# Kernel tuning notes

Hardware: AMD Instinct MI355X
Metric: run time of the kernel (lower is better)

## Reference

```python
import jax, jax.numpy as jnp
import numpy as np

L = 2          # num_blocks
E = 256        # embed_features
FIN = 64       # input_features
FF = 4 * E     # dim_feedforward
OUT = 10       # out_dim
WCTX = 64      # context_len
B, S = 2, 1024
LN_EPS = 1e-5


def _ln(x, g, b):
    m = jnp.mean(x, axis=-1, keepdims=True)
    v = jnp.mean((x - m) ** 2, axis=-1, keepdims=True)
    return (x - m) / jnp.sqrt(v + LN_EPS) * g + b


def setup_inputs() -> dict:
    key = jax.random.key(0)
    ks = jax.random.split(key, 12)
    s = 0.02
    return {
        "inputs": jax.random.normal(ks[0], (B, S, FIN), jnp.float32),
        "embed_w": jax.random.normal(ks[1], (E, FIN), jnp.float32) * s,
        "embed_b": jnp.zeros((E,), jnp.float32),
        "qkv_w": jax.random.normal(ks[2], (L, 3 * E, E), jnp.float32) * s,
        "qkv_b": jnp.zeros((L, 3 * E), jnp.float32),
        "attn_out_w": jax.random.normal(ks[3], (L, E, E), jnp.float32) * s,
        "attn_out_b": jnp.zeros((L, E), jnp.float32),
        "ln1_g": jnp.ones((L, E), jnp.float32),
        "ln1_b": jnp.zeros((L, E), jnp.float32),
        "ffn1_w": jax.random.normal(ks[4], (L, FF, E), jnp.float32) * s,
        "ffn1_b": jnp.zeros((L, FF), jnp.float32),
        "ffn2_w": jax.random.normal(ks[5], (L, E, FF), jnp.float32) * s,
        "ffn2_b": jnp.zeros((L, E), jnp.float32),
        "ln2_g": jnp.ones((L, E), jnp.float32),
        "ln2_b": jnp.zeros((L, E), jnp.float32),
        "head_w": jax.random.normal(ks[6], (OUT, E), jnp.float32) * s,
        "head_b": jnp.zeros((OUT,), jnp.float32),
        "context_len": WCTX,
    }


def reference(inputs, embed_w, embed_b, qkv_w, qkv_b, attn_out_w, attn_out_b,
              ln1_g, ln1_b, ffn1_w, ffn1_b, ffn2_w, ffn2_b, ln2_g, ln2_b,
              head_w, head_b, context_len):
    b, s, _ = inputs.shape
    e = embed_w.shape[0]
    nh = max(1, e // 64) * 2           # torch: nhead = max(1, E//64)*2
    hd = e // nh
    scale = 1.0 / np.sqrt(hd)
    w = context_len

    emb = inputs @ embed_w.T + embed_b                       # [B,S,E]
    # left-pad with W-1 zeros so window pos p = padded[p:p+W] (zeros for early pos)
    padded = jnp.pad(emb, ((0, 0), (w - 1, 0), (0, 0)))
    idx = jnp.arange(s)[:, None] + jnp.arange(w)[None, :]    # [S,W]
    x = padded[:, idx].reshape(b * s, w, e)                  # [B*S,W,E]

    nlayers = qkv_w.shape[0]
    for l in range(nlayers):
        qkv = x @ qkv_w[l].T + qkv_b[l]                      # [N,W,3E]
        q, k, v = jnp.split(qkv, 3, axis=-1)
        q = q.reshape(-1, w, nh, hd)
        k = k.reshape(-1, w, nh, hd)
        v = v.reshape(-1, w, nh, hd)
        scores = jnp.einsum('nqhd,nkhd->nhqk', q, k) * scale
        attn = jax.nn.softmax(scores, axis=-1)
        o = jnp.einsum('nhqk,nkhd->nqhd', attn, v).reshape(-1, w, e)
        o = o @ attn_out_w[l].T + attn_out_b[l]
        x = _ln(x + o, ln1_g[l], ln1_b[l])                   # post-norm (torch default)
        ff = jax.nn.silu(x @ ffn1_w[l].T + ffn1_b[l]) @ ffn2_w[l].T + ffn2_b[l]
        x = _ln(x + ff, ln2_g[l], ln2_b[l])

    out = x[:, -1, :] @ head_w.T + head_b                    # last token of each window
    return out.reshape(b, s, -1)
```

## Files before the change

kernel.cpp:

```cpp
#include <hip/hip_runtime.h>
#include <hip/hip_bf16.h>

#define BB_ 2
#define SS_ 1024
#define FIN_ 64
#define EE_ 256
#define FF_ 1024
#define NH_ 8
#define HD_ 32
#define OUT_ 10
#define NWIN (BB_ * SS_)
#define NT 512
#define SCALE_ 0.17677669529663687f
#define XBP 264
#define TPAD 1088

typedef unsigned short u16;
typedef unsigned int u32;
typedef __attribute__((ext_vector_type(8))) short bf8_t;
typedef __attribute__((ext_vector_type(4))) float f4_t;
#define MFMA_B16(a, b, c) __builtin_amdgcn_mfma_f32_16x16x32_bf16(a, b, c, 0, 0, 0)

__device__ __forceinline__ u16 bf16r(float f) {
    u32 u = __builtin_bit_cast(u32, f);
    return (u16)((u + 0x7FFFu + ((u >> 16) & 1u)) >> 16);
}
__device__ __forceinline__ u32 pk_bf16(float a, float b) {
    return (u32)bf16r(a) | ((u32)bf16r(b) << 16);
}
__device__ __forceinline__ float b2f(u16 h) {
    return __builtin_bit_cast(float, ((u32)h) << 16);
}
__device__ __forceinline__ float b2f_lo(u32 u) {
    return __builtin_bit_cast(float, u << 16);
}
__device__ __forceinline__ float b2f_hi(u32 u) {
    return __builtin_bit_cast(float, u & 0xFFFF0000u);
}

__device__ __forceinline__ float dot4(float4 a, float4 b) {
    return a.x * b.x + a.y * b.y + a.z * b.z + a.w * b.w;
}
__device__ __forceinline__ float wsum(float v) {
#pragma unroll
    for (int o = 32; o > 0; o >>= 1) v += __shfl_xor(v, o, 64);
    return v;
}
__device__ __forceinline__ float wmax(float v) {
#pragma unroll
    for (int o = 32; o > 0; o >>= 1) v = fmaxf(v, __shfl_xor(v, o, 64));
    return v;
}
__device__ __forceinline__ float silu_f(float h) { return h / (1.f + __expf(-h)); }

struct CvtArgs {
    const float* s[9];
    u16* d[9];
    int n[9];
};

__global__ void k_pre(const float* __restrict__ in, const float* __restrict__ embw,
                      const float* __restrict__ embb, const float* __restrict__ qkv_b,
                      CvtArgs ca, float* __restrict__ emb, u16* __restrict__ qkvp) {
    __shared__ float row[FIN_];
    const int blk = blockIdx.x;
    const int tid = threadIdx.x;
    if (blk < 2048) {
        if (tid < FIN_) row[tid] = in[blk * FIN_ + tid];
        __syncthreads();
        const float4* w4 = (const float4*)(embw + tid * FIN_);
        const float4* r4 = (const float4*)row;
        float s = 0.f;
#pragma unroll
        for (int c = 0; c < FIN_ / 4; ++c) s += dot4(w4[c], r4[c]);
        emb[blk * EE_ + tid] = s + embb[tid];
    } else if (blk < 2816) {
        const int b2 = blk - 2048;
#pragma unroll 1
        for (int seg = 0; seg < 9; ++seg) {
            const float* __restrict__ src = ca.s[seg];
            u16* __restrict__ dst = ca.d[seg];
            const int nn = ca.n[seg];
            for (int i = b2 * 256 + tid; i < nn; i += 768 * 256)
                dst[i] = bf16r(src[i]);
        }
    } else {
        const int b3 = blk - 2816;
        for (int f = b3 * 256 + tid; f < 2 * 64 * 768; f += 8 * 256) {
            const int bat = f / 49152;
            const int rem = f - bat * 49152;
            const int r = rem / 768, cl = rem - r * 768;
            qkvp[((size_t)bat * TPAD + r) * 768 + cl] = bf16r(qkv_b[cl]);
        }
    }
}

__global__ __launch_bounds__(512) void k_qkv0m(const float* __restrict__ emb,
                                               const u16* __restrict__ wq0b,
                                               const float* __restrict__ qkvb,
                                               u16* __restrict__ qkvp) {
    __shared__ u16 ab[16 * XBP];
    const int b = blockIdx.x;
    const int tid = threadIdx.x, lane = tid & 63, wv = tid >> 6;
    const int col = lane & 15, quad = lane >> 4;
    for (int idx = tid; idx < 16 * 256; idx += 512) {
        const int i = idx >> 8, e = idx & 255;
        ab[i * XBP + e] = bf16r(emb[(b * 16 + i) * EE_ + e]);
    }
    __syncthreads();
    f4_t acc[6];
#pragma unroll
    for (int nt = 0; nt < 6; ++nt) acc[nt] = (f4_t){0.f, 0.f, 0.f, 0.f};
#pragma unroll
    for (int ks = 0; ks < 8; ++ks) {
        const bf8_t ax = *(const bf8_t*)(ab + col * XBP + ks * 32 + quad * 8);
#pragma unroll
        for (int nt = 0; nt < 6; ++nt) {
            const int r = wv * 96 + nt * 16 + col;
            const bf8_t bw = *(const bf8_t*)(wq0b + r * EE_ + ks * 32 + quad * 8);
            acc[nt] = MFMA_B16(ax, bw, acc[nt]);
        }
    }
#pragma unroll
    for (int nt = 0; nt < 6; ++nt) {
        const int cc = wv * 96 + nt * 16 + col;
        const float bs = qkvb[cc];
#pragma unroll
        for (int j = 0; j < 4; ++j) {
            const int tok = b * 16 + quad * 4 + j;
            const int bb = tok >> 10;
            const size_t ti = (size_t)bb * TPAD + (tok & 1023) + 64;
            qkvp[ti * 768 + cc] = bf16r(acc[nt][j] + bs);
        }
    }
}

__device__ __forceinline__ void reg_ln(float (&x)[2][4][4], float* red, float* stat,
                                       u16* xb,
                                       float gc0, float gc1, float bc0, float bc1,
                                       int tid, int wv, int col, int quad,
                                       int colg0, int colg1) {
    float ps[4][4], pq[4][4];
#pragma unroll
    for (int mt = 0; mt < 4; ++mt)
#pragma unroll
        for (int j = 0; j < 4; ++j) {
            const float v0 = x[0][mt][j], v1 = x[1][mt][j];
            ps[mt][j] = v0 + v1;
            pq[mt][j] = v0 * v0 + v1 * v1;
        }
#pragma unroll
    for (int o = 1; o < 16; o <<= 1) {
#pragma unroll
        for (int mt = 0; mt < 4; ++mt)
#pragma unroll
            for (int j = 0; j < 4; ++j) {
                ps[mt][j] += __shfl_xor(ps[mt][j], o);
                pq[mt][j] += __shfl_xor(pq[mt][j], o);
            }
    }
    if (col == 0) {
#pragma unroll
        for (int mt = 0; mt < 4; ++mt)
#pragma unroll
            for (int j = 0; j < 4; ++j) {
                const int row = mt * 16 + quad * 4 + j;
                red[row * 17 + wv * 2] = ps[mt][j];
                red[row * 17 + wv * 2 + 1] = pq[mt][j];
            }
    }
    __syncthreads();
    if (tid < 64) {
        float s = 0.f, q = 0.f;
#pragma unroll
        for (int w = 0; w < 8; ++w) {
            s += red[tid * 17 + w * 2];
            q += red[tid * 17 + w * 2 + 1];
        }
        const float m = s * 0.00390625f;
        const float var = q * 0.00390625f - m * m;
        stat[tid * 2] = m;
        stat[tid * 2 + 1] = rsqrtf(var + 1e-5f);
    }
    __syncthreads();
#pragma unroll
    for (int mt = 0; mt < 4; ++mt)
#pragma unroll
        for (int j = 0; j < 4; ++j) {
            const int row = mt * 16 + quad * 4 + j;
            const float m = stat[row * 2];
            const float rs = stat[row * 2 + 1];
            const float xn0 = (x[0][mt][j] - m) * rs * gc0 + bc0;
            const float xn1 = (x[1][mt][j] - m) * rs * gc1 + bc1;
            x[0][mt][j] = xn0;
            x[1][mt][j] = xn1;
            const u32 w = pk_bf16(xn0, xn1);
            xb[row * XBP + colg0] = (u16)w;
            xb[row * XBP + colg1] = (u16)(w >> 16);
        }
}

struct __align__(16) SMemA {
    union {
        struct { u16 qkpb[9216]; u16 vt[4608]; } att;
        struct { float red[64 * 17]; float stat[128]; } ln;
    } r1;
    u16 obxb[64 * XBP];
};

__global__ __launch_bounds__(NT, 4) void k_attn(
    const float* __restrict__ emb, const u16* __restrict__ qkvp,
    const u16* __restrict__ wob, const float* __restrict__ aob,
    const float* __restrict__ ln1g, const float* __restrict__ ln1b,
    u16* __restrict__ xbg) {
    __shared__ SMemA sm;
    const int n = blockIdx.x;
    const int bb = n >> 10, p = n & 1023;
    const int tid = threadIdx.x;
    const int lane = tid & 63, wv = tid >> 6;
    const int col = lane & 15, quad = lane >> 4;
    const int colg0 = wv * 32 + col, colg1 = colg0 + 16;

    for (int hp = 0; hp < 4; ++hp) {
        {
            const int i = tid >> 3, dg = tid & 7;
            const size_t rb = ((size_t)bb * TPAD + (p + 1 + i)) * 768 + hp * 64 + dg * 8;
            const uint4 q4 = *(const uint4*)(qkvp + rb);
            const uint4 k4 = *(const uint4*)(qkvp + rb + 256);
            const uint4 v4 = *(const uint4*)(qkvp + rb + 512);
            *(uint4*)(sm.r1.att.qkpb + i * 72 + dg * 8) = q4;
            *(uint4*)(sm.r1.att.qkpb + 4608 + i * 72 + dg * 8) = k4;
            union { uint4 u; u16 h[8]; } vu; vu.u = v4;
#pragma unroll
            for (int c = 0; c < 8; ++c)
                sm.r1.att.vt[(dg * 8 + c) * 72 + i] = vu.h[c];
        }
        __syncthreads();
        const int hh = wv >> 2, mt_ = wv & 3;
        const int r0 = mt_ * 16 + quad * 4;
        const bf8_t aq = *(const bf8_t*)(sm.r1.att.qkpb + (mt_ * 16 + col) * 72 + hh * 32 + quad * 8);
        f4_t sc[4];
#pragma unroll
        for (int nt = 0; nt < 4; ++nt) {
            const bf8_t bk = *(const bf8_t*)(sm.r1.att.qkpb + 4608 + (nt * 16 + col) * 72 + hh * 32 + quad * 8);
            f4_t z = {0.f, 0.f, 0.f, 0.f};
            sc[nt] = MFMA_B16(aq, bk, z);
        }
#pragma unroll
        for (int j = 0; j < 4; ++j) {
            float s0 = sc[0][j] * SCALE_, s1 = sc[1][j] * SCALE_;
            float s2v = sc[2][j] * SCALE_, s3 = sc[3][j] * SCALE_;
            float m = fmaxf(fmaxf(s0, s1), fmaxf(s2v, s3));
            m = fmaxf(m, __shfl_xor(m, 1)); m = fmaxf(m, __shfl_xor(m, 2));
            m = fmaxf(m, __shfl_xor(m, 4)); m = fmaxf(m, __shfl_xor(m, 8));
            const float e0 = __expf(s0 - m), e1 = __expf(s1 - m);
            const float e2 = __expf(s2v - m), e3 = __expf(s3 - m);
            float s = e0 + e1 + e2 + e3;
            s += __shfl_xor(s, 1); s += __shfl_xor(s, 2);
            s += __shfl_xor(s, 4); s += __shfl_xor(s, 8);
            const float inv = 1.f / s;
            sc[0][j] = e0 * inv; sc[1][j] = e1 * inv;
            sc[2][j] = e2 * inv; sc[3][j] = e3 * inv;
        }
        __syncthreads();
        u16* pbh = sm.r1.att.qkpb + hh * 4608;
#pragma unroll
        for (int nt = 0; nt < 4; ++nt) {
            const u32 w01 = pk_bf16(sc[nt][0], sc[nt][1]);
            const u32 w23 = pk_bf16(sc[nt][2], sc[nt][3]);
            u16* pp = pbh + r0 * 72 + nt * 16 + col;
            pp[0] = (u16)w01; pp[72] = (u16)(w01 >> 16);
            pp[144] = (u16)w23; pp[216] = (u16)(w23 >> 16);
        }
        f4_t ov[2];
        ov[0] = (f4_t){0.f, 0.f, 0.f, 0.f}; ov[1] = (f4_t){0.f, 0.f, 0.f, 0.f};
#pragma unroll
        for (int ks = 0; ks < 2; ++ks) {
            const bf8_t ap = *(const bf8_t*)(pbh + (mt_ * 16 + col) * 72 + ks * 32 + quad * 8);
#pragma unroll
            for (int ntl = 0; ntl < 2; ++ntl) {
                const bf8_t bv = *(const bf8_t*)(sm.r1.att.vt +
                                                 (hh * 32 + ntl * 16 + col) * 72 + ks * 32 + quad * 8);
                ov[ntl] = MFMA_B16(ap, bv, ov[ntl]);
            }
        }
#pragma unroll
        for (int ntl = 0; ntl < 2; ++ntl) {
            const u32 w01 = pk_bf16(ov[ntl][0], ov[ntl][1]);
            const u32 w23 = pk_bf16(ov[ntl][2], ov[ntl][3]);
            u16* oo = sm.obxb + r0 * XBP + (hp * 2 + hh) * 32 + ntl * 16 + col;
            oo[0] = (u16)w01; oo[XBP] = (u16)(w01 >> 16);
            oo[2 * XBP] = (u16)w23; oo[3 * XBP] = (u16)(w23 >> 16);
        }
        __syncthreads();
    }

    f4_t pacc[2][4];
#pragma unroll
    for (int a = 0; a < 2; ++a)
#pragma unroll
        for (int m = 0; m < 4; ++m) pacc[a][m] = (f4_t){0.f, 0.f, 0.f, 0.f};
#pragma unroll 2
    for (int ks = 0; ks < 8; ++ks) {
        bf8_t ao[4];
#pragma unroll
        for (int mt = 0; mt < 4; ++mt)
            ao[mt] = *(const bf8_t*)(sm.obxb + (mt * 16 + col) * XBP + ks * 32 + quad * 8);
#pragma unroll
        for (int ntl = 0; ntl < 2; ++ntl) {
            const bf8_t bw = *(const bf8_t*)(wob + ((wv * 2 + ntl) * 16 + col) * EE_ +
                                             ks * 32 + quad * 8);
#pragma unroll
            for (int mt = 0; mt < 4; ++mt) pacc[ntl][mt] = MFMA_B16(ao[mt], bw, pacc[ntl][mt]);
        }
    }

    const float aob_0 = aob[colg0], aob_1 = aob[colg1];
    float x[2][4][4];
#pragma unroll
    for (int mt = 0; mt < 4; ++mt)
#pragma unroll
        for (int j = 0; j < 4; ++j) {
            const int row = mt * 16 + quad * 4 + j;
            const int t = p - 63 + row;
            const size_t base = (size_t)((bb << 10) + t) * EE_;
            const float e0 = (t >= 0) ? emb[base + colg0] : 0.f;
            const float e1 = (t >= 0) ? emb[base + colg1] : 0.f;
            x[0][mt][j] = e0 + aob_0 + pacc[0][mt][j];
            x[1][mt][j] = e1 + aob_1 + pacc[1][mt][j];
        }
    __syncthreads();
    reg_ln(x, sm.r1.ln.red, sm.r1.ln.stat, sm.obxb,
           ln1g[colg0], ln1g[colg1], ln1b[colg0], ln1b[colg1],
           tid, wv, col, quad, colg0, colg1);
    __syncthreads();
    u16* dst = xbg + (size_t)n * 64 * 256;
#pragma unroll
    for (int k = 0; k < 4; ++k) {
        const int idx = tid + k * NT;
        const int row = idx >> 5, seg = idx & 31;
        *(uint4*)(dst + row * 256 + seg * 8) = *(const uint4*)(sm.obxb + row * XBP + seg * 8);
    }
}

struct __align__(16) SMemB {
    u16 xb[64 * XBP];
    union {
        u16 hb[64 * 136];
        struct { u16 k1[64 * 66]; u16 v1[64 * 66]; } kv;
        struct { float red[64 * 17]; float stat[128]; } ln;
    } c;
    float x1row[256];
    float o1b[256];
    float q1b[64];
    float sbuf2[128];
};

__global__ __launch_bounds__(NT, 4) void k_mlp(
    const u16* __restrict__ xbg,
    const u16* __restrict__ w1b, const u16* __restrict__ w2b,
    const u16* __restrict__ wkvb, const u16* __restrict__ wq1b,
    const u16* __restrict__ wob1,
    const float* __restrict__ qkv_b, const float* __restrict__ aob,
    const float* __restrict__ f1b, const float* __restrict__ f2b,
    const float* __restrict__ ln2g, const float* __restrict__ ln2b,
    float* __restrict__ x2g) {
    __shared__ SMemB sm;
    const int n = blockIdx.x;
    const int tid = threadIdx.x;
    const int lane = tid & 63, wv = tid >> 6;
    const int col = lane & 15, quad = lane >> 4;
    const int colg0 = wv * 32 + col, colg1 = colg0 + 16;

    const float* qkv_b1 = qkv_b + 3 * EE_;
    const float* aob1p = aob + EE_;

    const u16* src = xbg + (size_t)n * 64 * 256;
#pragma unroll
    for (int k = 0; k < 4; ++k) {
        const int idx = tid + k * NT;
        const int row = idx >> 5, seg = idx & 31;
        *(uint4*)(sm.xb + row * XBP + seg * 8) = *(const uint4*)(src + row * 256 + seg * 8);
    }
    __syncthreads();

    f4_t facc[2][4];
#pragma unroll
    for (int a = 0; a < 2; ++a)
#pragma unroll
        for (int m = 0; m < 4; ++m) facc[a][m] = (f4_t){0.f, 0.f, 0.f, 0.f};

    for (int c = 0; c < 8; ++c) {
        {
            f4_t hacc[4];
#pragma unroll
            for (int m = 0; m < 4; ++m) hacc[m] = (f4_t){0.f, 0.f, 0.f, 0.f};
            const int f = c * 128 + wv * 16 + col;
#pragma unroll 2
            for (int ks = 0; ks < 8; ++ks) {
                const bf8_t bw = *(const bf8_t*)(w1b + f * EE_ + ks * 32 + quad * 8);
#pragma unroll
                for (int mt = 0; mt < 4; ++mt) {
                    const bf8_t axr = *(const bf8_t*)(sm.xb + (mt * 16 + col) * XBP + ks * 32 + quad * 8);
                    hacc[mt] = MFMA_B16(axr, bw, hacc[mt]);
                }
            }
            const float bv = f1b[f];
            const int lc = wv * 16 + col;
#pragma unroll
            for (int mt = 0; mt < 4; ++mt) {
                const u32 w01 = pk_bf16(silu_f(hacc[mt][0] + bv), silu_f(hacc[mt][1] + bv));
                const u32 w23 = pk_bf16(silu_f(hacc[mt][2] + bv), silu_f(hacc[mt][3] + bv));
                u16* hh2 = sm.c.hb + (mt * 16 + quad * 4) * 136 + lc;
                hh2[0] = (u16)w01; hh2[136] = (u16)(w01 >> 16);
                hh2[272] = (u16)w23; hh2[408] = (u16)(w23 >> 16);
            }
        }
        __syncthreads();
        {
#pragma unroll 2
            for (int ks = 0; ks < 4; ++ks) {
                bf8_t ah[4];
#pragma unroll
                for (int mt = 0; mt < 4; ++mt)
                    ah[mt] = *(const bf8_t*)(sm.c.hb + (mt * 16 + col) * 136 + ks * 32 + quad * 8);
#pragma unroll
                for (int ntl = 0; ntl < 2; ++ntl) {
                    const int e = (wv * 2 + ntl) * 16 + col;
                    const bf8_t bw = *(const bf8_t*)(w2b + e * FF_ + c * 128 + ks * 32 + quad * 8);
#pragma unroll
                    for (int mt = 0; mt < 4; ++mt) facc[ntl][mt] = MFMA_B16(ah[mt], bw, facc[ntl][mt]);
                }
            }
        }
        __syncthreads();
    }
    const float f2b_0 = f2b[colg0], f2b_1 = f2b[colg1];
    float x[2][4][4];
#pragma unroll
    for (int mt = 0; mt < 4; ++mt)
#pragma unroll
        for (int j = 0; j < 4; ++j) {
            const int row = mt * 16 + quad * 4 + j;
            x[0][mt][j] = b2f(sm.xb[row * XBP + colg0]) + facc[0][mt][j] + f2b_0;
            x[1][mt][j] = b2f(sm.xb[row * XBP + colg1]) + facc[1][mt][j] + f2b_1;
        }
    __syncthreads();
    reg_ln(x, sm.c.ln.red, sm.c.ln.stat, sm.xb,
           ln2g[colg0], ln2g[colg1], ln2b[colg0], ln2b[colg1],
           tid, wv, col, quad, colg0, colg1);
    if (quad == 3) {
        sm.x1row[colg0] = x[0][3][3];
        sm.x1row[colg1] = x[1][3][3];
    }
    __syncthreads();

    for (int hp = 0; hp < 4; ++hp) {
        {
            const int hf = wv >> 2, mtk = wv & 3;
            f4_t kacc[4];
#pragma unroll
            for (int a = 0; a < 4; ++a) kacc[a] = (f4_t){0.f, 0.f, 0.f, 0.f};
#pragma unroll 2
            for (int ks = 0; ks < 8; ++ks) {
                const bf8_t ax = *(const bf8_t*)(sm.xb + (mtk * 16 + col) * XBP + ks * 32 + quad * 8);
#pragma unroll
                for (int nt = 0; nt < 4; ++nt) {
                    const int wr = hf * EE_ + hp * 64 + nt * 16 + col;
                    const bf8_t bw = *(const bf8_t*)(wkvb + wr * EE_ + ks * 32 + quad * 8);
                    kacc[nt] = MFMA_B16(ax, bw, kacc[nt]);
                }
            }
            u16* dst = hf ? sm.c.kv.v1 : sm.c.kv.k1;
#pragma unroll
            for (int nt = 0; nt < 4; ++nt) {
                const int cc = nt * 16 + col;
                const float bs = qkv_b1[(hf + 1) * EE_ + hp * 64 + cc];
                const u32 w01 = pk_bf16(kacc[nt][0] + bs, kacc[nt][1] + bs);
                const u32 w23 = pk_bf16(kacc[nt][2] + bs, kacc[nt][3] + bs);
                u16* dd = dst + (mtk * 16 + quad * 4) * 66 + cc;
                dd[0] = (u16)w01; dd[66] = (u16)(w01 >> 16);
                dd[132] = (u16)w23; dd[198] = (u16)(w23 >> 16);
            }
        }
        if (tid < 64) {
            const u16* wq = wq1b + (hp * 64 + tid) * EE_;
            float s = 0.f;
#pragma unroll 8
            for (int k2 = 0; k2 < 128; ++k2) {
                const u32 u = *(const u32*)(wq + k2 * 2);
                s += sm.x1row[2 * k2] * b2f_lo(u) + sm.x1row[2 * k2 + 1] * b2f_hi(u);
            }
            sm.q1b[tid] = s + qkv_b1[hp * 64 + tid];
        }
        __syncthreads();
        if (tid < 128) {
            const int hh = tid >> 6, jj = tid & 63;
            const u16* kr = sm.c.kv.k1 + jj * 66 + hh * 32;
            const float* qv = sm.q1b + hh * 32;
            float s = 0.f;
#pragma unroll
            for (int d = 0; d < 32; ++d) s += qv[d] * b2f(kr[d]);
            s *= SCALE_;
            const float m = wmax(s);
            const float e = __expf(s - m);
            const float su = wsum(e);
            sm.sbuf2[tid] = e / su;
        }
        __syncthreads();
        if (tid < 64) {
            const int hh = tid >> 5, d = tid & 31;
            float acc = 0.f;
            for (int j = 0; j < 64; ++j)
                acc += sm.sbuf2[hh * 64 + j] * b2f(sm.c.kv.v1[j * 66 + hh * 32 + d]);
            sm.o1b[hp * 64 + hh * 32 + d] = acc;
        }
        __syncthreads();
    }

    if (tid < 256) {
        const u16* wr = wob1 + tid * EE_;
        float s = 0.f;
#pragma unroll 8
        for (int k2 = 0; k2 < 128; ++k2) {
            const u32 u = *(const u32*)(wr + k2 * 2);
            s += sm.o1b[2 * k2] * b2f_lo(u) + sm.o1b[2 * k2 + 1] * b2f_hi(u);
        }
        x2g[n * EE_ + tid] = sm.x1row[tid] + s + aob1p[tid];
    }
}

__global__ __launch_bounds__(256) void k_tail(
    const float* __restrict__ x2g, const u16* __restrict__ w1b1,
    const float* __restrict__ f1b1, const u16* __restrict__ w2b1,
    const float* __restrict__ f2b1, const float* __restrict__ g1,
    const float* __restrict__ b1, const float* __restrict__ g2,
    const float* __restrict__ b2, const float* __restrict__ hw,
    const float* __restrict__ hbb, float* __restrict__ out) {
    __shared__ float xa[4 * 260];
    __shared__ float hid[4 * 1024];
    const int tid = threadIdx.x, lane = tid & 63, w = tid >> 6;
    const int n0 = blockIdx.x * 4;
    {
        const float* src = x2g + (size_t)(n0 + w) * EE_;
        const float v0 = src[lane], v1 = src[lane + 64], v2 = src[lane + 128], v3 = src[lane + 192];
        const float m = wsum(v0 + v1 + v2 + v3) * 0.00390625f;
        const float d0 = v0 - m, d1 = v1 - m, d2 = v2 - m, d3 = v3 - m;
        const float var = wsum(d0 * d0 + d1 * d1 + d2 * d2 + d3 * d3) * 0.00390625f;
        const float rs = rsqrtf(var + 1e-5f);
        xa[w * 260 + lane] = d0 * rs * g1[lane] + b1[lane];
        xa[w * 260 + lane + 64] = d1 * rs * g1[lane + 64] + b1[lane + 64];
        xa[w * 260 + lane + 128] = d2 * rs * g1[lane + 128] + b1[lane + 128];
        xa[w * 260 + lane + 192] = d3 * rs * g1[lane + 192] + b1[lane + 192];
    }
    __syncthreads();
#pragma unroll 1
    for (int r = 0; r < 4; ++r) {
        const int f = r * 256 + tid;
        const u16* wrow = w1b1 + f * EE_;
        float a0 = 0.f, a1 = 0.f, a2 = 0.f, a3 = 0.f;
#pragma unroll 4
        for (int k2 = 0; k2 < 128; ++k2) {
            const u32 u = *(const u32*)(wrow + k2 * 2);
            const float lo = b2f_lo(u), hi = b2f_hi(u);
            const float2 h0 = *(const float2*)(xa + 0 * 260 + k2 * 2);
            const float2 h1 = *(const float2*)(xa + 1 * 260 + k2 * 2);
            const float2 h2 = *(const float2*)(xa + 2 * 260 + k2 * 2);
            const float2 h3 = *(const float2*)(xa + 3 * 260 + k2 * 2);
            a0 += h0.x * lo + h0.y * hi;
            a1 += h1.x * lo + h1.y * hi;
            a2 += h2.x * lo + h2.y * hi;
            a3 += h3.x * lo + h3.y * hi;
        }
        const float bv = f1b1[f];
        hid[0 * 1024 + f] = silu_f(a0 + bv);
        hid[1 * 1024 + f] = silu_f(a1 + bv);
        hid[2 * 1024 + f] = silu_f(a2 + bv);
        hid[3 * 1024 + f] = silu_f(a3 + bv);
    }
    __syncthreads();
    {
        const u16* wrow = w2b1 + tid * FF_;
        float a0 = 0.f, a1 = 0.f, a2 = 0.f, a3 = 0.f;
#pragma unroll 4
        for (int k2 = 0; k2 < 512; ++k2) {
            const u32 u = *(const u32*)(wrow + k2 * 2);
            const float lo = b2f_lo(u), hi = b2f_hi(u);
            const float2 h0 = *(const float2*)(hid + 0 * 1024 + k2 * 2);
            const float2 h1 = *(const float2*)(hid + 1 * 1024 + k2 * 2);
            const float2 h2 = *(const float2*)(hid + 2 * 1024 + k2 * 2);
            const float2 h3 = *(const float2*)(hid + 3 * 1024 + k2 * 2);
            a0 += h0.x * lo + h0.y * hi;
            a1 += h1.x * lo + h1.y * hi;
            a2 += h2.x * lo + h2.y * hi;
            a3 += h3.x * lo + h3.y * hi;
        }
        const float bv = f2b1[tid];
        const float r0 = xa[0 * 260 + tid] + a0 + bv;
        const float r1 = xa[1 * 260 + tid] + a1 + bv;
        const float r2 = xa[2 * 260 + tid] + a2 + bv;
        const float r3 = xa[3 * 260 + tid] + a3 + bv;
        __syncthreads();
        xa[0 * 260 + tid] = r0;
        xa[1 * 260 + tid] = r1;
        xa[2 * 260 + tid] = r2;
        xa[3 * 260 + tid] = r3;
    }
    __syncthreads();
    {
        float* row = xa + w * 260;
        const float v0 = row[lane], v1 = row[lane + 64], v2 = row[lane + 128], v3 = row[lane + 192];
        const float m = wsum(v0 + v1 + v2 + v3) * 0.00390625f;
        const float d0 = v0 - m, d1 = v1 - m, d2 = v2 - m, d3 = v3 - m;
        const float var = wsum(d0 * d0 + d1 * d1 + d2 * d2 + d3 * d3) * 0.00390625f;
        const float rs = rsqrtf(var + 1e-5f);
        __syncthreads();
        row[lane] = d0 * rs * g2[lane] + b2[lane];
        row[lane + 64] = d1 * rs * g2[lane + 64] + b2[lane + 64];
        row[lane + 128] = d2 * rs * g2[lane + 128] + b2[lane + 128];
        row[lane + 192] = d3 * rs * g2[lane + 192] + b2[lane + 192];
    }
    __syncthreads();
    if (tid < 4 * OUT_) {
        const int win = tid / OUT_, o = tid % OUT_;
        const float* wr = hw + o * EE_;
        const float* xr = xa + win * 260;
        float s = 0.f;
#pragma unroll 8
        for (int c4 = 0; c4 < 64; ++c4)
            s += dot4(*(const float4*)(xr + c4 * 4), *(const float4*)(wr + c4 * 4));
        out[(n0 + win) * OUT_ + o] = s + hbb[o];
    }
}

extern "C" void kernel_launch(void* const* d_in, const int* in_sizes, int n_in,
                              void* d_out, int out_size, void* d_ws, size_t ws_size,
                              hipStream_t stream) {
    (void)in_sizes; (void)n_in; (void)out_size; (void)ws_size;
    const float* inputs = (const float*)d_in[0];
    const float* embed_w = (const float*)d_in[1];
    const float* embed_b = (const float*)d_in[2];
    const float* qkv_w = (const float*)d_in[3];
    const float* qkv_b = (const float*)d_in[4];
    const float* attn_out_w = (const float*)d_in[5];
    const float* attn_out_b = (const float*)d_in[6];
    const float* ln1_g = (const float*)d_in[7];
    const float* ln1_b = (const float*)d_in[8];
    const float* ffn1_w = (const float*)d_in[9];
    const float* ffn1_b = (const float*)d_in[10];
    const float* ffn2_w = (const float*)d_in[11];
    const float* ffn2_b = (const float*)d_in[12];
    const float* ln2_g = (const float*)d_in[13];
    const float* ln2_b = (const float*)d_in[14];
    const float* head_w = (const float*)d_in[15];
    const float* head_b = (const float*)d_in[16];
    float* out = (float*)d_out;

    char* wsb = (char*)d_ws;
    size_t off = 0;
    auto alloc = [&](size_t bytes) { char* pp = wsb + off; off += (bytes + 511) & ~511ull; return pp; };
    float* emb   = (float*)alloc((size_t)NWIN * EE_ * 4);
    u16*   qkvp  = (u16*)alloc((size_t)BB_ * TPAD * 768 * 2);
    u16*   xbg   = (u16*)alloc((size_t)NWIN * 64 * 256 * 2);
    float* x2g   = (float*)alloc((size_t)NWIN * EE_ * 4);
    u16*   w1b   = (u16*)alloc(FF_ * EE_ * 2);
    u16*   w2b   = (u16*)alloc(EE_ * FF_ * 2);
    u16*   wob   = (u16*)alloc(EE_ * EE_ * 2);
    u16*   wkvb  = (u16*)alloc(2 * EE_ * EE_ * 2);
    u16*   w1b1  = (u16*)alloc(FF_ * EE_ * 2);
    u16*   w2b1  = (u16*)alloc(EE_ * FF_ * 2);
    u16*   wob1  = (u16*)alloc(EE_ * EE_ * 2);
    u16*   wq1b  = (u16*)alloc(EE_ * EE_ * 2);
    u16*   wq0b  = (u16*)alloc(3 * EE_ * EE_ * 2);

    CvtArgs ca;
    ca.s[0] = ffn1_w;                            ca.d[0] = w1b;  ca.n[0] = FF_ * EE_;
    ca.s[1] = ffn2_w;                            ca.d[1] = w2b;  ca.n[1] = EE_ * FF_;
    ca.s[2] = attn_out_w;                        ca.d[2] = wob;  ca.n[2] = EE_ * EE_;
    ca.s[3] = qkv_w + 3 * EE_ * EE_ + EE_ * EE_; ca.d[3] = wkvb; ca.n[3] = 2 * EE_ * EE_;
    ca.s[4] = ffn1_w + FF_ * EE_;                ca.d[4] = w1b1; ca.n[4] = FF_ * EE_;
    ca.s[5] = ffn2_w + EE_ * FF_;                ca.d[5] = w2b1; ca.n[5] = EE_ * FF_;
    ca.s[6] = attn_out_w + EE_ * EE_;            ca.d[6] = wob1; ca.n[6] = EE_ * EE_;
    ca.s[7] = qkv_w + 3 * EE_ * EE_;             ca.d[7] = wq1b; ca.n[7] = EE_ * EE_;
    ca.s[8] = qkv_w;                             ca.d[8] = wq0b; ca.n[8] = 3 * EE_ * EE_;

    k_pre<<<2824, 256, 0, stream>>>(inputs, embed_w, embed_b, qkv_b, ca, emb, qkvp);
    k_qkv0m<<<NWIN / 16, 512, 0, stream>>>(emb, wq0b, qkv_b, qkvp);
    k_attn<<<NWIN, NT, 0, stream>>>(emb, qkvp, wob, attn_out_b, ln1_g, ln1_b, xbg);
    k_mlp<<<NWIN, NT, 0, stream>>>(xbg, w1b, w2b, wkvb, wq1b, wob1,
                                   qkv_b, attn_out_b, ffn1_b, ffn2_b,
                                   ln2_g, ln2_b, x2g);
    k_tail<<<NWIN / 4, 256, 0, stream>>>(x2g, w1b1, ffn1_b + FF_, w2b1, ffn2_b + EE_,
                                         ln1_g + EE_, ln1_b + EE_, ln2_g + EE_, ln2_b + EE_,
                                         head_w, head_b, out);
}
```

Baseline: 968.5 us.

## Double-buffer FFN hidden tiles, batch layer-2 KV heads, separate attention P buffer

The FFN loop now double-buffers the hidden tile, so FFN1 for chunk c+1 is computed before FFN2 for chunk c. This removes one barrier per chunk and lets MFMA work from the two stages interleave. The second-layer K/V/attention stage processes two head pairs per iteration (2 chunks instead of 4), with each wave covering two row tiles, and all 256 q values are computed up front. The attention kernel writes probabilities into a dedicated pb buffer instead of reusing the qk buffer, which removes a barrier, at the cost of more LDS per block and possibly lower occupancy.

```diff
diff --git a/kernel.cpp b/kernel.cpp
--- a/kernel.cpp
+++ b/kernel.cpp
@@ -202,7 +202,7 @@
 
 struct __align__(16) SMemA {
     union {
-        struct { u16 qkpb[9216]; u16 vt[4608]; } att;
+        struct { u16 qkpb[9216]; u16 vt[4608]; u16 pb[9216]; } att;
         struct { float red[64 * 17]; float stat[128]; } ln;
     } r1;
     u16 obxb[64 * XBP];
@@ -262,8 +262,7 @@
             sc[0][j] = e0 * inv; sc[1][j] = e1 * inv;
             sc[2][j] = e2 * inv; sc[3][j] = e3 * inv;
         }
-        __syncthreads();
-        u16* pbh = sm.r1.att.qkpb + hh * 4608;
+        u16* pbh = sm.r1.att.pb + hh * 4608;
 #pragma unroll
         for (int nt = 0; nt < 4; ++nt) {
             const u32 w01 = pk_bf16(sc[nt][0], sc[nt][1]);
@@ -346,14 +345,14 @@
 struct __align__(16) SMemB {
     u16 xb[64 * XBP];
     union {
-        u16 hb[64 * 136];
-        struct { u16 k1[64 * 66]; u16 v1[64 * 66]; } kv;
+        u16 hb2[2][64 * 136];
+        u16 kvb[4 * 64 * 66];
         struct { float red[64 * 17]; float stat[128]; } ln;
     } c;
     float x1row[256];
     float o1b[256];
-    float q1b[64];
-    float sbuf2[128];
+    float q1b[256];
+    float sbuf2[256];
 };
 
 __global__ __launch_bounds__(NT, 4) void k_mlp(
@@ -390,51 +389,59 @@
 #pragma unroll
         for (int m = 0; m < 4; ++m) facc[a][m] = (f4_t){0.f, 0.f, 0.f, 0.f};
 
+    auto ffn1_step = [&](int c) {
+        f4_t hacc[4];
+#pragma unroll
+        for (int m = 0; m < 4; ++m) hacc[m] = (f4_t){0.f, 0.f, 0.f, 0.f};
+        const int f = c * 128 + wv * 16 + col;
+#pragma unroll 2
+        for (int ks = 0; ks < 8; ++ks) {
+            const bf8_t bw = *(const bf8_t*)(w1b + f * EE_ + ks * 32 + quad * 8);
+#pragma unroll
+            for (int mt = 0; mt < 4; ++mt) {
+                const bf8_t axr = *(const bf8_t*)(sm.xb + (mt * 16 + col) * XBP + ks * 32 + quad * 8);
+                hacc[mt] = MFMA_B16(axr, bw, hacc[mt]);
+            }
+        }
+        const float bv = f1b[f];
+        const int lc = wv * 16 + col;
+        u16* hbc = sm.c.hb2[c & 1];
+#pragma unroll
+        for (int mt = 0; mt < 4; ++mt) {
+            const u32 w01 = pk_bf16(silu_f(hacc[mt][0] + bv), silu_f(hacc[mt][1] + bv));
+            const u32 w23 = pk_bf16(silu_f(hacc[mt][2] + bv), silu_f(hacc[mt][3] + bv));
+            u16* hh2 = hbc + (mt * 16 + quad * 4) * 136 + lc;
+            hh2[0] = (u16)w01; hh2[136] = (u16)(w01 >> 16);
+            hh2[272] = (u16)w23; hh2[408] = (u16)(w23 >> 16);
+        }
+    };
+    auto ffn2_step = [&](int c) {
+        const u16* hbc = sm.c.hb2[c & 1];
+#pragma unroll 2
+        for (int ks = 0; ks < 4; ++ks) {
+            bf8_t ah[4];
+#pragma unroll
+            for (int mt = 0; mt < 4; ++mt)
+                ah[mt] = *(const bf8_t*)(hbc + (mt * 16 + col) * 136 + ks * 32 + quad * 8);
+#pragma unroll
+            for (int ntl = 0; ntl < 2; ++ntl) {
+                const int e = (wv * 2 + ntl) * 16 + col;
+                const bf8_t bw = *(const bf8_t*)(w2b + e * FF_ + c * 128 + ks * 32 + quad * 8);
+#pragma unroll
+                for (int mt = 0; mt < 4; ++mt) facc[ntl][mt] = MFMA_B16(ah[mt], bw, facc[ntl][mt]);
+            }
+        }
+    };
+
+    ffn1_step(0);
+    __syncthreads();
+#pragma unroll 1
     for (int c = 0; c < 8; ++c) {
-        {
-            f4_t hacc[4];
-#pragma unroll
-            for (int m = 0; m < 4; ++m) hacc[m] = (f4_t){0.f, 0.f, 0.f, 0.f};
-            const int f = c * 128 + wv * 16 + col;
-#pragma unroll 2
-            for (int ks = 0; ks < 8; ++ks) {
-                const bf8_t bw = *(const bf8_t*)(w1b + f * EE_ + ks * 32 + quad * 8);
-#pragma unroll
-                for (int mt = 0; mt < 4; ++mt) {
-                    const bf8_t axr = *(const bf8_t*)(sm.xb + (mt * 16 + col) * XBP + ks * 32 + quad * 8);
-                    hacc[mt] = MFMA_B16(axr, bw, hacc[mt]);
-                }
-            }
-            const float bv = f1b[f];
-            const int lc = wv * 16 + col;
-#pragma unroll
-            for (int mt = 0; mt < 4; ++mt) {
-                const u32 w01 = pk_bf16(silu_f(hacc[mt][0] + bv), silu_f(hacc[mt][1] + bv));
-                const u32 w23 = pk_bf16(silu_f(hacc[mt][2] + bv), silu_f(hacc[mt][3] + bv));
-                u16* hh2 = sm.c.hb + (mt * 16 + quad * 4) * 136 + lc;
-                hh2[0] = (u16)w01; hh2[136] = (u16)(w01 >> 16);
-                hh2[272] = (u16)w23; hh2[408] = (u16)(w23 >> 16);
-            }
-        }
-        __syncthreads();
-        {
-#pragma unroll 2
-            for (int ks = 0; ks < 4; ++ks) {
-                bf8_t ah[4];
-#pragma unroll
-                for (int mt = 0; mt < 4; ++mt)
-                    ah[mt] = *(const bf8_t*)(sm.c.hb + (mt * 16 + col) * 136 + ks * 32 + quad * 8);
-#pragma unroll
-                for (int ntl = 0; ntl < 2; ++ntl) {
-                    const int e = (wv * 2 + ntl) * 16 + col;
-                    const bf8_t bw = *(const bf8_t*)(w2b + e * FF_ + c * 128 + ks * 32 + quad * 8);
-#pragma unroll
-                    for (int mt = 0; mt < 4; ++mt) facc[ntl][mt] = MFMA_B16(ah[mt], bw, facc[ntl][mt]);
-                }
-            }
-        }
-        __syncthreads();
-    }
+        if (c < 7) ffn1_step(c + 1);
+        ffn2_step(c);
+        __syncthreads();
+    }
+
     const float f2b_0 = f2b[colg0], f2b_1 = f2b[colg1];
     float x[2][4][4];
 #pragma unroll
@@ -455,49 +462,60 @@
     }
     __syncthreads();
 
-    for (int hp = 0; hp < 4; ++hp) {
+#pragma unroll 1
+    for (int chunk = 0; chunk < 2; ++chunk) {
         {
-            const int hf = wv >> 2, mtk = wv & 3;
-            f4_t kacc[4];
-#pragma unroll
-            for (int a = 0; a < 4; ++a) kacc[a] = (f4_t){0.f, 0.f, 0.f, 0.f};
+            const int hpc = wv & 1, hf = (wv >> 1) & 1, mtkh = (wv >> 2) & 1;
+            const int hpg = chunk * 2 + hpc;
+            f4_t kacc[2][4];
+#pragma unroll
+            for (int a = 0; a < 2; ++a)
+#pragma unroll
+                for (int b = 0; b < 4; ++b) kacc[a][b] = (f4_t){0.f, 0.f, 0.f, 0.f};
 #pragma unroll 2
             for (int ks = 0; ks < 8; ++ks) {
-                const bf8_t ax = *(const bf8_t*)(sm.xb + (mtk * 16 + col) * XBP + ks * 32 + quad * 8);
+                bf8_t ax[2];
+#pragma unroll
+                for (int m2 = 0; m2 < 2; ++m2)
+                    ax[m2] = *(const bf8_t*)(sm.xb + ((mtkh * 2 + m2) * 16 + col) * XBP + ks * 32 + quad * 8);
 #pragma unroll
                 for (int nt = 0; nt < 4; ++nt) {
-                    const int wr = hf * EE_ + hp * 64 + nt * 16 + col;
+                    const int wr = hf * EE_ + hpg * 64 + nt * 16 + col;
                     const bf8_t bw = *(const bf8_t*)(wkvb + wr * EE_ + ks * 32 + quad * 8);
-                    kacc[nt] = MFMA_B16(ax, bw, kacc[nt]);
+#pragma unroll
+                    for (int m2 = 0; m2 < 2; ++m2) kacc[m2][nt] = MFMA_B16(ax[m2], bw, kacc[m2][nt]);
                 }
             }
-            u16* dst = hf ? sm.c.kv.v1 : sm.c.kv.k1;
-#pragma unroll
-            for (int nt = 0; nt < 4; ++nt) {
-                const int cc = nt * 16 + col;
-                const float bs = qkv_b1[(hf + 1) * EE_ + hp * 64 + cc];
-                const u32 w01 = pk_bf16(kacc[nt][0] + bs, kacc[nt][1] + bs);
-                const u32 w23 = pk_bf16(kacc[nt][2] + bs, kacc[nt][3] + bs);
-                u16* dd = dst + (mtk * 16 + quad * 4) * 66 + cc;
-                dd[0] = (u16)w01; dd[66] = (u16)(w01 >> 16);
-                dd[132] = (u16)w23; dd[198] = (u16)(w23 >> 16);
-            }
-        }
-        if (tid < 64) {
-            const u16* wq = wq1b + (hp * 64 + tid) * EE_;
+            u16* dst = sm.c.kvb + (hpc * 2 + hf) * 4224;
+#pragma unroll
+            for (int m2 = 0; m2 < 2; ++m2)
+#pragma unroll
+                for (int nt = 0; nt < 4; ++nt) {
+                    const int cc = nt * 16 + col;
+                    const float bs = qkv_b1[(hf + 1) * EE_ + hpg * 64 + cc];
+                    const u32 w01 = pk_bf16(kacc[m2][nt][0] + bs, kacc[m2][nt][1] + bs);
+                    const u32 w23 = pk_bf16(kacc[m2][nt][2] + bs, kacc[m2][nt][3] + bs);
+                    u16* dd = dst + ((mtkh * 2 + m2) * 16 + quad * 4) * 66 + cc;
+                    dd[0] = (u16)w01; dd[66] = (u16)(w01 >> 16);
+                    dd[132] = (u16)w23; dd[198] = (u16)(w23 >> 16);
+                }
+        }
+        if (chunk == 0 && tid < 256) {
+            const u16* wq = wq1b + tid * EE_;
             float s = 0.f;
 #pragma unroll 8
             for (int k2 = 0; k2 < 128; ++k2) {
                 const u32 u = *(const u32*)(wq + k2 * 2);
                 s += sm.x1row[2 * k2] * b2f_lo(u) + sm.x1row[2 * k2 + 1] * b2f_hi(u);
             }
-            sm.q1b[tid] = s + qkv_b1[hp * 64 + tid];
-        }
-        __syncthreads();
-        if (tid < 128) {
-            const int hh = tid >> 6, jj = tid & 63;
-            const u16* kr = sm.c.kv.k1 + jj * 66 + hh * 32;
-            const float* qv = sm.q1b + hh * 32;
+            sm.q1b[tid] = s + qkv_b1[tid];
+        }
+        __syncthreads();
+        if (tid < 256) {
+            const int hc = tid >> 6, jj = tid & 63;
+            const int hpc = hc >> 1, hh = hc & 1;
+            const u16* kr = sm.c.kvb + (hpc * 2) * 4224 + jj * 66 + hh * 32;
+            const float* qv = sm.q1b + (chunk * 4 + hc) * 32;
             float s = 0.f;
 #pragma unroll
             for (int d = 0; d < 32; ++d) s += qv[d] * b2f(kr[d]);
@@ -505,15 +523,17 @@
             const float m = wmax(s);
             const float e = __expf(s - m);
             const float su = wsum(e);
-            sm.sbuf2[tid] = e / su;
-        }
-        __syncthreads();
-        if (tid < 64) {
-            const int hh = tid >> 5, d = tid & 31;
+            sm.sbuf2[hc * 64 + jj] = e / su;
+        }
+        __syncthreads();
+        if (tid < 128) {
+            const int hc = tid >> 5, d = tid & 31;
+            const int hpc = hc >> 1, hh = hc & 1;
+            const u16* vr = sm.c.kvb + (hpc * 2 + 1) * 4224 + hh * 32 + d;
             float acc = 0.f;
             for (int j = 0; j < 64; ++j)
-                acc += sm.sbuf2[hh * 64 + j] * b2f(sm.c.kv.v1[j * 66 + hh * 32 + d]);
-            sm.o1b[hp * 64 + hh * 32 + d] = acc;
+                acc += sm.sbuf2[hc * 64 + j] * b2f(vr[j * 66]);
+            sm.o1b[(chunk * 4 + hc) * 32 + d] = acc;
         }
         __syncthreads();
     }
```

After: 795.6 us. 1.22x faster.
